# Kernel optimization log

Hardware: AMD Instinct MI355X
Metric: run time of the kernel (lower is better)

## Reference

```python
import jax, jax.numpy as jnp
import numpy as np

B, S, D, P = 16, 128, 768, 1024
N_CLASSES = 121  # dataset != 'restaurant'


def setup_inputs() -> dict:
    key = jax.random.key(0)
    ks = jax.random.split(key, 8)
    scale = lambda fan_in: 1.0 / np.sqrt(fan_in)
    return {
        "spans_embedding": jax.random.normal(ks[0], (B, S, D), dtype=jnp.float32),
        "W1": jax.random.normal(ks[1], (3 * D, 2 * D), dtype=jnp.float32) * scale(3 * D),
        "b1": jnp.zeros((2 * D,), dtype=jnp.float32),
        "W2": jax.random.normal(ks[2], (2 * D, D), dtype=jnp.float32) * scale(2 * D),
        "b2": jnp.zeros((D,), dtype=jnp.float32),
        "W3": jax.random.normal(ks[3], (D, N_CLASSES), dtype=jnp.float32) * scale(D),
        "b3": jnp.zeros((N_CLASSES,), dtype=jnp.float32),
        "span_masks": jnp.ones((B, S), dtype=jnp.int32),
        "batch_idx": jax.random.randint(ks[4], (P,), 0, B, dtype=jnp.int64),
        "aspect_idx": jax.random.randint(ks[5], (P,), 0, S - 2, dtype=jnp.int64),
        "opinion_idx": jax.random.randint(ks[6], (P,), 0, S - 2, dtype=jnp.int64),
    }


def reference(spans_embedding, W1, b1, W2, b2, W3, b3,
              span_masks, batch_idx, aspect_idx, opinion_idx):
    S_ = spans_embedding.shape[1]
    pos = jnp.arange(S_)
    last = jnp.sum(span_masks, axis=1) - 1          # [B] last valid span index
    li = last[batch_idx]                             # [P]
    emb = spans_embedding[batch_idx]                 # [P, S, D] gathered per pair

    def rng_max(lo, hi):                             # max over spans in [lo, hi)
        mask = (pos[None, :] >= lo[:, None]) & (pos[None, :] < hi[:, None])
        return jnp.max(jnp.where(mask[:, :, None], emb, -jnp.inf), axis=1)

    def rng_mean(lo, hi):                            # mean over spans in [lo, hi)
        m = ((pos[None, :] >= lo[:, None]) & (pos[None, :] < hi[:, None])).astype(emb.dtype)
        cnt = jnp.maximum(jnp.sum(m, axis=1), 1.0)
        return jnp.einsum('ps,psd->pd', m, emb) / cnt[:, None]

    ones = jnp.ones_like(aspect_idx)
    # boundary index b: aspect when aspect!=0, else opinion (matches all non-both-zero branches)
    b = jnp.where(aspect_idx != 0, aspect_idx, opinion_idx)
    emb0 = spans_embedding[batch_idx, 0]             # [P, D]
    embL = spans_embedding[batch_idx, li]            # [P, D]
    left_nz = jnp.where((b == 1)[:, None], emb0, rng_max(ones, b))
    right_nz = jnp.where((b == li)[:, None], embL, rng_max(b, li))

    both0 = (aspect_idx == 0) & (opinion_idx == 0)
    left = jnp.where(both0[:, None], rng_mean(ones, li), left_nz)
    right = jnp.where(both0[:, None], rng_max(ones, li), right_nz)

    aspect_rep = spans_embedding[batch_idx, aspect_idx]
    o_eff = jnp.where(opinion_idx == 0, li, opinion_idx)
    opinion_rep = spans_embedding[batch_idx, o_eff]

    x = jnp.concatenate([aspect_rep + opinion_rep, left, right], axis=1)  # [P, 3D]
    h = jax.nn.relu(x @ W1 + b1)
    h = jax.nn.relu(h @ W2 + b2)
    return h @ W3 + b3                               # [P, n_classes]
```

## Files before the change

kernel.cpp:

```cpp
#include <hip/hip_runtime.h>
#include <hip/hip_bf16.h>
#include <math.h>

#define S_LEN 128
#define D_DIM 768
#define P_PAIRS 1024
#define B_BATCH 16

typedef __attribute__((ext_vector_type(8))) short bf16x8;
typedef __attribute__((ext_vector_type(4))) float f32x4;

#define PB_UNITS (B_BATCH * (D_DIM / 64))
#define T1_UNITS ((2304 / 64) * (1536 / 64))
#define T2_UNITS ((1536 / 64) * (768 / 64))
#define T3_UNITS ((768 / 64) * (128 / 64))

union SmemU {
    struct {
        ushort semb[128][64];
        ushort spref[128][64];
        ushort ssuf[128][64];
        ushort smean[64];
        float  lred[3][4][64];
        int    li;
    } pb;
    float t64[64][65];
};

__device__ __forceinline__ ushort f2bf(float f) {
    __hip_bfloat16 h = __float2bfloat16(f);
    return *(ushort*)&h;
}

__device__ __forceinline__ float bf2f(ushort u) {
    unsigned int x = ((unsigned int)u) << 16;
    float f;
    __builtin_memcpy(&f, &x, 4);
    return f;
}

__device__ __forceinline__ void gload16(const void* g, void* l) {
    __builtin_amdgcn_global_load_lds(
        (const __attribute__((address_space(1))) void*)g,
        (__attribute__((address_space(3))) void*)l, 16, 0, 0);
}

__global__ __launch_bounds__(256) void fused_prep_kernel(
    const float* __restrict__ emb_all,
    const int* __restrict__ span_masks,
    const int* __restrict__ batch_idx,
    const int* __restrict__ aspect_idx,
    const int* __restrict__ opinion_idx,
    ushort* __restrict__ X,
    const float* __restrict__ W1, ushort* __restrict__ W1t,
    const float* __restrict__ W2, ushort* __restrict__ W2t,
    const float* __restrict__ W3, ushort* __restrict__ W3t)
{
    __shared__ SmemU sm;
    int bid = blockIdx.x;
    int tid = threadIdx.x;

    if (bid < PB_UNITS) {
        int b = bid / (D_DIM / 64);
        int chunk = bid % (D_DIM / 64);
        int lane = tid & 63;
        int g = tid >> 6;
        int r0 = g * 32;
        int col = chunk * 64 + lane;

        if (tid == 0) {
            int s = 0;
            for (int i = 0; i < S_LEN; ++i) s += span_masks[b * S_LEN + i];
            sm.pb.li = s - 1;
        }
        __syncthreads();
        int li = sm.pb.li;

        const float* embb = emb_all + (size_t)b * S_LEN * D_DIM;

        float v[32];
        #pragma unroll
        for (int r = 0; r < 32; ++r) {
            v[r] = embb[(size_t)(r0 + r) * D_DIM + col];
            sm.pb.semb[r0 + r][lane] = f2bf(v[r]);
        }

        float wmax = -INFINITY, umax = -INFINITY, s = 0.f;
        #pragma unroll
        for (int r = 0; r < 32; ++r) {
            int gr = r0 + r;
            wmax = fmaxf(wmax, (gr == 0) ? -INFINITY : v[r]);
            bool in = (gr >= 1) && (gr < li);
            umax = fmaxf(umax, in ? v[r] : -INFINITY);
            s += in ? v[r] : 0.f;
        }
        sm.pb.lred[0][g][lane] = wmax;
        sm.pb.lred[1][g][lane] = umax;
        sm.pb.lred[2][g][lane] = s;
        __syncthreads();

        float basep = -INFINITY;
        #pragma unroll
        for (int gg = 0; gg < 3; ++gg)
            if (gg < g) basep = fmaxf(basep, sm.pb.lred[0][gg][lane]);
        float bases = -INFINITY;
        #pragma unroll
        for (int gg = 1; gg < 4; ++gg)
            if (gg > g) bases = fmaxf(bases, sm.pb.lred[1][gg][lane]);

        if (g == 0) {
            float tot = sm.pb.lred[2][0][lane] + sm.pb.lred[2][1][lane]
                      + sm.pb.lred[2][2][lane] + sm.pb.lred[2][3][lane];
            int cnt = (li - 1) > 0 ? (li - 1) : 1;
            sm.pb.smean[lane] = f2bf(tot / (float)cnt);
        }

        float m = basep;
        #pragma unroll
        for (int r = 0; r < 32; ++r) {
            int gr = r0 + r;
            m = fmaxf(m, (gr == 0) ? -INFINITY : v[r]);
            sm.pb.spref[gr][lane] = f2bf(m);
        }
        float m2 = bases;
        #pragma unroll
        for (int r = 31; r >= 0; --r) {
            int gr = r0 + r;
            bool in = (gr >= 1) && (gr < li);
            m2 = fmaxf(m2, in ? v[r] : -INFINITY);
            if (gr >= 1) sm.pb.ssuf[gr][lane] = f2bf(m2);
        }
        __syncthreads();

        int pbase = g * 256;
        for (int c = 0; c < 256; c += 64) {
            int p = pbase + c + lane;
            int vb = batch_idx[p];
            int va = aspect_idx[p];
            int vo = opinion_idx[p];
            unsigned long long mask = __ballot(vb == b);
            while (mask) {
                int i = __ffsll((long long)mask) - 1;
                mask &= mask - 1;
                int pp = pbase + c + i;
                int a = __shfl(va, i);
                int o = __shfl(vo, i);
                bool both0 = (a == 0) && (o == 0);
                int bnd = (a != 0) ? a : o;
                int oe = (o == 0) ? li : o;
                float ar  = bf2f(sm.pb.semb[a][lane]);
                float orp = bf2f(sm.pb.semb[oe][lane]);
                ushort left, right;
                if (both0) {
                    left  = sm.pb.smean[lane];
                    right = sm.pb.spref[li - 1][lane];
                } else {
                    left  = (bnd == 1)  ? sm.pb.semb[0][lane]
                                        : sm.pb.spref[bnd - 1][lane];
                    right = (bnd == li) ? sm.pb.semb[li][lane]
                                        : sm.pb.ssuf[bnd][lane];
                }
                size_t base = (size_t)pp * (3 * D_DIM) + col;
                X[base]             = f2bf(ar + orp);
                X[base + D_DIM]     = left;
                X[base + 2 * D_DIM] = right;
            }
        }
    } else {
        int tb = bid - PB_UNITS;
        const float* in; ushort* out; int K, N, Npad, bx, by;
        if (tb < T1_UNITS) {
            in = W1; out = W1t; K = 2304; N = 1536; Npad = 1536;
            bx = tb % (2304 / 64); by = tb / (2304 / 64);
        } else if (tb < T1_UNITS + T2_UNITS) {
            tb -= T1_UNITS;
            in = W2; out = W2t; K = 1536; N = 768; Npad = 768;
            bx = tb % (1536 / 64); by = tb / (1536 / 64);
        } else {
            tb -= T1_UNITS + T2_UNITS;
            in = W3; out = W3t; K = 768; N = 121; Npad = 128;
            bx = tb % (768 / 64); by = tb / (768 / 64);
        }
        int k0 = bx * 64, n0 = by * 64;

        int kr = tid >> 2;
        int nq = (tid & 3) * 16;
        if (n0 + 64 <= N) {
            #pragma unroll
            for (int j = 0; j < 4; ++j) {
                float4 vv = *(const float4*)&in[(size_t)(k0 + kr) * N + n0 + nq + j * 4];
                *(float4*)&sm.t64[kr][nq + j * 4] = vv;
            }
        } else {
            #pragma unroll
            for (int j = 0; j < 16; ++j) {
                int n = n0 + nq + j;
                sm.t64[kr][nq + j] = (n < N) ? in[(size_t)(k0 + kr) * N + n] : 0.f;
            }
        }
        __syncthreads();

        int nr = tid >> 2;
        int kq = (tid & 3) * 16;
        if (n0 + nr < Npad) {
            ushort tmp[16];
            #pragma unroll
            for (int j = 0; j < 16; ++j) tmp[j] = f2bf(sm.t64[kq + j][nr]);
            ushort* dst = out + (size_t)(n0 + nr) * K + k0 + kq;
            *(bf16x8*)dst       = *(bf16x8*)&tmp[0];
            *(bf16x8*)(dst + 8) = *(bf16x8*)&tmp[8];
        }
    }
}

template<int WRITE_BF16, int RELU>
__global__ __launch_bounds__(256, 2) void gemm_mfma(
    const ushort* __restrict__ A,
    const ushort* __restrict__ Bt,
    const float* __restrict__ bias,
    void* __restrict__ Cout,
    int M, int N, int K)
{
    __shared__ ushort lds[4][128 * 64];
    int tid = threadIdx.x;
    int lane = tid & 63;
    int w = tid >> 6;
    int wr = w >> 1, wc = w & 1;
    int rowBase = blockIdx.y * 64;
    int colBase = blockIdx.x * 64;

    int srow  = lane >> 3;
    int scolb = (((lane & 7) ^ srow) << 4);
    const char* Abase = (const char*)(A  + (size_t)rowBase * K);
    const char* Bbase = (const char*)(Bt + (size_t)colBase * K);
    size_t rstride = (size_t)K * 2;

    f32x4 acc[2][2] = {};
    int nt = K >> 6;

    auto stage = [&](int buf, int t) {
        size_t kb0 = (size_t)t << 7;
        #pragma unroll
        for (int i = 0; i < 2; ++i) {
            int r = w * 16 + i * 8 + srow;
            gload16(Abase + (size_t)r * rstride + kb0 + scolb,
                    &lds[buf][(w * 16 + i * 8) * 64]);
        }
        #pragma unroll
        for (int i = 0; i < 2; ++i) {
            int r = w * 16 + i * 8 + srow;
            gload16(Bbase + (size_t)r * rstride + kb0 + scolb,
                    &lds[buf][(64 + w * 16 + i * 8) * 64]);
        }
    };

    stage(0, 0);
    stage(1, 1);
    stage(2, 2);

    for (int t = 0; t < nt; ++t) {
        int cur = t & 3;
        int ahead = nt - 1 - t;
        if (ahead >= 2)      asm volatile("s_waitcnt vmcnt(8)" ::: "memory");
        else if (ahead == 1) asm volatile("s_waitcnt vmcnt(4)" ::: "memory");
        else                 asm volatile("s_waitcnt vmcnt(0)" ::: "memory");
        __builtin_amdgcn_s_barrier();
        __builtin_amdgcn_sched_barrier(0);

        if (t + 3 < nt) stage((t + 3) & 3, t + 3);

        const char* lb = (const char*)&lds[cur][0];
        int kq = (lane >> 4) << 4;
        bf16x8 af[2][2], bfr[2][2];
        #pragma unroll
        for (int m = 0; m < 2; ++m) {
            int row = wr * 32 + m * 16 + (lane & 15);
            #pragma unroll
            for (int kk = 0; kk < 2; ++kk) {
                int addr = row * 128 + ((kq + kk * 64) ^ ((row & 7) << 4));
                af[m][kk] = *(const bf16x8*)(lb + addr);
            }
        }
        #pragma unroll
        for (int n = 0; n < 2; ++n) {
            int row = 64 + wc * 32 + n * 16 + (lane & 15);
            #pragma unroll
            for (int kk = 0; kk < 2; ++kk) {
                int addr = row * 128 + ((kq + kk * 64) ^ ((row & 7) << 4));
                bfr[n][kk] = *(const bf16x8*)(lb + addr);
            }
        }
        __builtin_amdgcn_s_setprio(1);
        #pragma unroll
        for (int m = 0; m < 2; ++m)
            #pragma unroll
            for (int n = 0; n < 2; ++n)
                #pragma unroll
                for (int kk = 0; kk < 2; ++kk)
                    acc[m][n] = __builtin_amdgcn_mfma_f32_16x16x32_bf16(
                        af[m][kk], bfr[n][kk], acc[m][n], 0, 0, 0);
        __builtin_amdgcn_s_setprio(0);
    }

    #pragma unroll
    for (int m = 0; m < 2; ++m) {
        #pragma unroll
        for (int n = 0; n < 2; ++n) {
            #pragma unroll
            for (int j = 0; j < 4; ++j) {
                int row = rowBase + wr * 32 + m * 16 + (lane >> 4) * 4 + j;
                int col = colBase + wc * 32 + n * 16 + (lane & 15);
                if (col < N && row < M) {
                    float v = acc[m][n][j] + bias[col];
                    if (RELU) v = fmaxf(v, 0.f);
                    if (WRITE_BF16)
                        ((ushort*)Cout)[(size_t)row * N + col] = f2bf(v);
                    else
                        ((float*)Cout)[(size_t)row * N + col] = v;
                }
            }
        }
    }
}

extern "C" void kernel_launch(void* const* d_in, const int* in_sizes, int n_in,
                              void* d_out, int out_size, void* d_ws, size_t ws_size,
                              hipStream_t stream) {
    const float* emb        = (const float*)d_in[0];
    const float* W1         = (const float*)d_in[1];
    const float* b1         = (const float*)d_in[2];
    const float* W2         = (const float*)d_in[3];
    const float* b2         = (const float*)d_in[4];
    const float* W3         = (const float*)d_in[5];
    const float* b3         = (const float*)d_in[6];
    const int* span_masks   = (const int*)d_in[7];
    const int* batch_idx    = (const int*)d_in[8];
    const int* aspect_idx   = (const int*)d_in[9];
    const int* opinion_idx  = (const int*)d_in[10];
    float* out = (float*)d_out;

    ushort* Xb  = (ushort*)d_ws;
    ushort* H2  = Xb;
    ushort* W1t = Xb  + (size_t)1024 * 2304;
    ushort* W2t = W1t + (size_t)1536 * 2304;
    ushort* W3t = W2t + (size_t)768 * 1536;
    ushort* H1  = W3t + (size_t)128 * 768;

    fused_prep_kernel<<<PB_UNITS + T1_UNITS + T2_UNITS + T3_UNITS, 256, 0, stream>>>(
        emb, span_masks, batch_idx, aspect_idx, opinion_idx, Xb,
        W1, W1t, W2, W2t, W3, W3t);

    gemm_mfma<1,1><<<dim3(1536/64, 1024/64), 256, 0, stream>>>(Xb, W1t, b1, H1, 1024, 1536, 2304);
    gemm_mfma<1,1><<<dim3( 768/64, 1024/64), 256, 0, stream>>>(H1, W2t, b2, H2, 1024, 768, 1536);
    gemm_mfma<0,0><<<dim3( 128/64, 1024/64), 256, 0, stream>>>(H2, W3t, b3, out, 1024, 121, 768);
}
```

Measured before the change: 55.15 us.

## Replace LDS-staged 4-wave GEMM with single-wave register-direct MFMA GEMM

Result: slower. 104.2 us (+89.0%).

```diff
diff --git a/kernel.cpp b/kernel.cpp
--- a/kernel.cpp
+++ b/kernel.cpp
@@ -37,12 +37,6 @@
     float f;
     __builtin_memcpy(&f, &x, 4);
     return f;
-}
-
-__device__ __forceinline__ void gload16(const void* g, void* l) {
-    __builtin_amdgcn_global_load_lds(
-        (const __attribute__((address_space(1))) void*)g,
-        (__attribute__((address_space(3))) void*)l, 16, 0, 0);
 }
 
 __global__ __launch_bounds__(256) void fused_prep_kernel(
@@ -214,102 +208,66 @@
 }
 
 template<int WRITE_BF16, int RELU>
-__global__ __launch_bounds__(256, 2) void gemm_mfma(
+__global__ __launch_bounds__(64) void gemm_direct(
     const ushort* __restrict__ A,
     const ushort* __restrict__ Bt,
     const float* __restrict__ bias,
     void* __restrict__ Cout,
     int M, int N, int K)
 {
-    __shared__ ushort lds[4][128 * 64];
-    int tid = threadIdx.x;
-    int lane = tid & 63;
-    int w = tid >> 6;
-    int wr = w >> 1, wc = w & 1;
-    int rowBase = blockIdx.y * 64;
-    int colBase = blockIdx.x * 64;
-
-    int srow  = lane >> 3;
-    int scolb = (((lane & 7) ^ srow) << 4);
-    const char* Abase = (const char*)(A  + (size_t)rowBase * K);
-    const char* Bbase = (const char*)(Bt + (size_t)colBase * K);
-    size_t rstride = (size_t)K * 2;
-
-    f32x4 acc[2][2] = {};
-    int nt = K >> 6;
-
-    auto stage = [&](int buf, int t) {
-        size_t kb0 = (size_t)t << 7;
-        #pragma unroll
-        for (int i = 0; i < 2; ++i) {
-            int r = w * 16 + i * 8 + srow;
-            gload16(Abase + (size_t)r * rstride + kb0 + scolb,
-                    &lds[buf][(w * 16 + i * 8) * 64]);
-        }
-        #pragma unroll
-        for (int i = 0; i < 2; ++i) {
-            int r = w * 16 + i * 8 + srow;
-            gload16(Bbase + (size_t)r * rstride + kb0 + scolb,
-                    &lds[buf][(64 + w * 16 + i * 8) * 64]);
-        }
-    };
-
-    stage(0, 0);
-    stage(1, 1);
-    stage(2, 2);
-
-    for (int t = 0; t < nt; ++t) {
-        int cur = t & 3;
-        int ahead = nt - 1 - t;
-        if (ahead >= 2)      asm volatile("s_waitcnt vmcnt(8)" ::: "memory");
-        else if (ahead == 1) asm volatile("s_waitcnt vmcnt(4)" ::: "memory");
-        else                 asm volatile("s_waitcnt vmcnt(0)" ::: "memory");
-        __builtin_amdgcn_s_barrier();
-        __builtin_amdgcn_sched_barrier(0);
-
-        if (t + 3 < nt) stage((t + 3) & 3, t + 3);
-
-        const char* lb = (const char*)&lds[cur][0];
-        int kq = (lane >> 4) << 4;
-        bf16x8 af[2][2], bfr[2][2];
-        #pragma unroll
-        for (int m = 0; m < 2; ++m) {
-            int row = wr * 32 + m * 16 + (lane & 15);
-            #pragma unroll
-            for (int kk = 0; kk < 2; ++kk) {
-                int addr = row * 128 + ((kq + kk * 64) ^ ((row & 7) << 4));
-                af[m][kk] = *(const bf16x8*)(lb + addr);
-            }
-        }
-        #pragma unroll
-        for (int n = 0; n < 2; ++n) {
-            int row = 64 + wc * 32 + n * 16 + (lane & 15);
-            #pragma unroll
-            for (int kk = 0; kk < 2; ++kk) {
-                int addr = row * 128 + ((kq + kk * 64) ^ ((row & 7) << 4));
-                bfr[n][kk] = *(const bf16x8*)(lb + addr);
-            }
-        }
-        __builtin_amdgcn_s_setprio(1);
-        #pragma unroll
-        for (int m = 0; m < 2; ++m)
-            #pragma unroll
-            for (int n = 0; n < 2; ++n)
-                #pragma unroll
-                for (int kk = 0; kk < 2; ++kk)
-                    acc[m][n] = __builtin_amdgcn_mfma_f32_16x16x32_bf16(
-                        af[m][kk], bfr[n][kk], acc[m][n], 0, 0, 0);
-        __builtin_amdgcn_s_setprio(0);
+    int lane = threadIdx.x;
+    int row0 = blockIdx.y * 64;
+    int col0 = blockIdx.x * 64;
+    int rl = lane & 15;
+    int kl = (lane >> 4) * 8;
+
+    const ushort* Ab = A  + (size_t)row0 * K + kl;
+    const ushort* Bb = Bt + (size_t)col0 * K + kl;
+
+    f32x4 acc[4][4] = {};
+    bf16x8 a0[4], b0[4], a1[4], b1[4], a2[4], b2[4];
+
+    #define LOADF(AS, BS, KO)                                                  \
+        do {                                                                   \
+            _Pragma("unroll")                                                  \
+            for (int f = 0; f < 4; ++f) {                                      \
+                AS[f] = *(const bf16x8*)(Ab + (size_t)(f * 16 + rl) * K + (KO)); \
+                BS[f] = *(const bf16x8*)(Bb + (size_t)(f * 16 + rl) * K + (KO)); \
+            }                                                                  \
+        } while (0)
+
+    #define MFMAS(AS, BS)                                                      \
+        do {                                                                   \
+            _Pragma("unroll")                                                  \
+            for (int m = 0; m < 4; ++m)                                        \
+                _Pragma("unroll")                                              \
+                for (int n = 0; n < 4; ++n)                                    \
+                    acc[m][n] = __builtin_amdgcn_mfma_f32_16x16x32_bf16(       \
+                        AS[m], BS[n], acc[m][n], 0, 0, 0);                     \
+        } while (0)
+
+    int nk = K >> 5;
+    LOADF(a0, b0, 0);
+    LOADF(a1, b1, 32);
+    for (int t = 0; t < nk; t += 3) {
+        if (t + 2 < nk) LOADF(a2, b2, (size_t)(t + 2) * 32);
+        MFMAS(a0, b0);
+        if (t + 3 < nk) LOADF(a0, b0, (size_t)(t + 3) * 32);
+        MFMAS(a1, b1);
+        if (t + 4 < nk) LOADF(a1, b1, (size_t)(t + 4) * 32);
+        MFMAS(a2, b2);
     }
+    #undef LOADF
+    #undef MFMAS
 
     #pragma unroll
-    for (int m = 0; m < 2; ++m) {
-        #pragma unroll
-        for (int n = 0; n < 2; ++n) {
+    for (int m = 0; m < 4; ++m) {
+        #pragma unroll
+        for (int n = 0; n < 4; ++n) {
             #pragma unroll
             for (int j = 0; j < 4; ++j) {
-                int row = rowBase + wr * 32 + m * 16 + (lane >> 4) * 4 + j;
-                int col = colBase + wc * 32 + n * 16 + (lane & 15);
+                int row = row0 + m * 16 + (lane >> 4) * 4 + j;
+                int col = col0 + n * 16 + rl;
                 if (col < N && row < M) {
                     float v = acc[m][n][j] + bias[col];
                     if (RELU) v = fmaxf(v, 0.f);
@@ -350,7 +308,7 @@
         emb, span_masks, batch_idx, aspect_idx, opinion_idx, Xb,
         W1, W1t, W2, W2t, W3, W3t);
 
-    gemm_mfma<1,1><<<dim3(1536/64, 1024/64), 256, 0, stream>>>(Xb, W1t, b1, H1, 1024, 1536, 2304);
-    gemm_mfma<1,1><<<dim3( 768/64, 1024/64), 256, 0, stream>>>(H1, W2t, b2, H2, 1024, 768, 1536);
-    gemm_mfma<0,0><<<dim3( 128/64, 1024/64), 256, 0, stream>>>(H2, W3t, b3, out, 1024, 121, 768);
-}
+    gemm_direct<1,1><<<dim3(1536/64, 1024/64), 64, 0, stream>>>(Xb, W1t, b1, H1, 1024, 1536, 2304);
+    gemm_direct<1,1><<<dim3( 768/64, 1024/64), 64, 0, stream>>>(H1, W2t, b2, H2, 1024, 768, 1536);
+    gemm_direct<0,0><<<dim3( 128/64, 1024/64), 64, 0, stream>>>(H2, W3t, b3, out, 1024, 121, 768);
+}
```

## Replace 4-wave GEMM blocks with single-wave 64x64 tiles and triple buffering

Applied to the files above, without the earlier changes.

Result: slower. 90.25 us (+63.7%).

```diff
diff --git a/kernel.cpp b/kernel.cpp
--- a/kernel.cpp
+++ b/kernel.cpp
@@ -214,102 +214,84 @@
 }
 
 template<int WRITE_BF16, int RELU>
-__global__ __launch_bounds__(256, 2) void gemm_mfma(
+__global__ __launch_bounds__(64) void gemm_sw(
     const ushort* __restrict__ A,
     const ushort* __restrict__ Bt,
     const float* __restrict__ bias,
     void* __restrict__ Cout,
     int M, int N, int K)
 {
-    __shared__ ushort lds[4][128 * 64];
-    int tid = threadIdx.x;
-    int lane = tid & 63;
-    int w = tid >> 6;
-    int wr = w >> 1, wc = w & 1;
-    int rowBase = blockIdx.y * 64;
-    int colBase = blockIdx.x * 64;
+    __shared__ ushort lds[3][128 * 64];
+    int lane = threadIdx.x;
+    int row0 = blockIdx.y * 64;
+    int col0 = blockIdx.x * 64;
+    int rl = lane & 15;
 
     int srow  = lane >> 3;
     int scolb = (((lane & 7) ^ srow) << 4);
-    const char* Abase = (const char*)(A  + (size_t)rowBase * K);
-    const char* Bbase = (const char*)(Bt + (size_t)colBase * K);
+    const char* Abase = (const char*)(A  + (size_t)row0 * K);
+    const char* Bbase = (const char*)(Bt + (size_t)col0 * K);
     size_t rstride = (size_t)K * 2;
 
-    f32x4 acc[2][2] = {};
+    f32x4 acc[4][4] = {};
     int nt = K >> 6;
 
     auto stage = [&](int buf, int t) {
         size_t kb0 = (size_t)t << 7;
         #pragma unroll
-        for (int i = 0; i < 2; ++i) {
-            int r = w * 16 + i * 8 + srow;
+        for (int i = 0; i < 8; ++i) {
+            int r = i * 8 + srow;
             gload16(Abase + (size_t)r * rstride + kb0 + scolb,
-                    &lds[buf][(w * 16 + i * 8) * 64]);
-        }
-        #pragma unroll
-        for (int i = 0; i < 2; ++i) {
-            int r = w * 16 + i * 8 + srow;
+                    &lds[buf][(i * 8) * 64]);
             gload16(Bbase + (size_t)r * rstride + kb0 + scolb,
-                    &lds[buf][(64 + w * 16 + i * 8) * 64]);
+                    &lds[buf][(64 + i * 8) * 64]);
         }
     };
 
     stage(0, 0);
     stage(1, 1);
-    stage(2, 2);
 
     for (int t = 0; t < nt; ++t) {
-        int cur = t & 3;
-        int ahead = nt - 1 - t;
-        if (ahead >= 2)      asm volatile("s_waitcnt vmcnt(8)" ::: "memory");
-        else if (ahead == 1) asm volatile("s_waitcnt vmcnt(4)" ::: "memory");
-        else                 asm volatile("s_waitcnt vmcnt(0)" ::: "memory");
-        __builtin_amdgcn_s_barrier();
+        int cur = t % 3;
+        if (t + 2 < nt) stage((t + 2) % 3, t + 2);
+        if (t + 2 < nt)      asm volatile("s_waitcnt vmcnt(32)" ::: "memory");
+        else if (t + 1 < nt) asm volatile("s_waitcnt vmcnt(16)" ::: "memory");
+        else                 asm volatile("s_waitcnt vmcnt(0)"  ::: "memory");
         __builtin_amdgcn_sched_barrier(0);
-
-        if (t + 3 < nt) stage((t + 3) & 3, t + 3);
 
         const char* lb = (const char*)&lds[cur][0];
         int kq = (lane >> 4) << 4;
-        bf16x8 af[2][2], bfr[2][2];
-        #pragma unroll
-        for (int m = 0; m < 2; ++m) {
-            int row = wr * 32 + m * 16 + (lane & 15);
-            #pragma unroll
-            for (int kk = 0; kk < 2; ++kk) {
-                int addr = row * 128 + ((kq + kk * 64) ^ ((row & 7) << 4));
-                af[m][kk] = *(const bf16x8*)(lb + addr);
-            }
-        }
-        #pragma unroll
-        for (int n = 0; n < 2; ++n) {
-            int row = 64 + wc * 32 + n * 16 + (lane & 15);
-            #pragma unroll
-            for (int kk = 0; kk < 2; ++kk) {
-                int addr = row * 128 + ((kq + kk * 64) ^ ((row & 7) << 4));
-                bfr[n][kk] = *(const bf16x8*)(lb + addr);
-            }
-        }
-        __builtin_amdgcn_s_setprio(1);
-        #pragma unroll
-        for (int m = 0; m < 2; ++m)
-            #pragma unroll
-            for (int n = 0; n < 2; ++n)
+        #pragma unroll
+        for (int kk = 0; kk < 2; ++kk) {
+            bf16x8 af[4], bfr[4];
+            #pragma unroll
+            for (int f = 0; f < 4; ++f) {
+                int ar = f * 16 + rl;
+                af[f]  = *(const bf16x8*)(lb + ar * 128 +
+                                          ((kq + kk * 64) ^ ((ar & 7) << 4)));
+                int br = 64 + f * 16 + rl;
+                bfr[f] = *(const bf16x8*)(lb + br * 128 +
+                                          ((kq + kk * 64) ^ ((br & 7) << 4)));
+            }
+            #pragma unroll
+            for (int m = 0; m < 4; ++m)
                 #pragma unroll
-                for (int kk = 0; kk < 2; ++kk)
+                for (int n = 0; n < 4; ++n)
                     acc[m][n] = __builtin_amdgcn_mfma_f32_16x16x32_bf16(
-                        af[m][kk], bfr[n][kk], acc[m][n], 0, 0, 0);
-        __builtin_amdgcn_s_setprio(0);
+                        af[m], bfr[n], acc[m][n], 0, 0, 0);
+        }
+        asm volatile("s_waitcnt lgkmcnt(0)" ::: "memory");
+        __builtin_amdgcn_sched_barrier(0);
     }
 
     #pragma unroll
-    for (int m = 0; m < 2; ++m) {
-        #pragma unroll
-        for (int n = 0; n < 2; ++n) {
+    for (int m = 0; m < 4; ++m) {
+        #pragma unroll
+        for (int n = 0; n < 4; ++n) {
             #pragma unroll
             for (int j = 0; j < 4; ++j) {
-                int row = rowBase + wr * 32 + m * 16 + (lane >> 4) * 4 + j;
-                int col = colBase + wc * 32 + n * 16 + (lane & 15);
+                int row = row0 + m * 16 + (lane >> 4) * 4 + j;
+                int col = col0 + n * 16 + rl;
                 if (col < N && row < M) {
                     float v = acc[m][n][j] + bias[col];
                     if (RELU) v = fmaxf(v, 0.f);
@@ -350,7 +332,7 @@
         emb, span_masks, batch_idx, aspect_idx, opinion_idx, Xb,
         W1, W1t, W2, W2t, W3, W3t);
 
-    gemm_mfma<1,1><<<dim3(1536/64, 1024/64), 256, 0, stream>>>(Xb, W1t, b1, H1, 1024, 1536, 2304);
-    gemm_mfma<1,1><<<dim3( 768/64, 1024/64), 256, 0, stream>>>(H1, W2t, b2, H2, 1024, 768, 1536);
-    gemm_mfma<0,0><<<dim3( 128/64, 1024/64), 256, 0, stream>>>(H2, W3t, b3, out, 1024, 121, 768);
-}
+    gemm_sw<1,1><<<dim3(1536/64, 1024/64), 64, 0, stream>>>(Xb, W1t, b1, H1, 1024, 1536, 2304);
+    gemm_sw<1,1><<<dim3( 768/64, 1024/64), 64, 0, stream>>>(H1, W2t, b2, H2, 1024, 768, 1536);
+    gemm_sw<0,0><<<dim3( 128/64, 1024/64), 64, 0, stream>>>(H2, W3t, b3, out, 1024, 121, 768);
+}
```
